# Kernel tuning notes

Measured on AMD Instinct MI355X. Metric: run time of the kernel, lower is better.

The kernel has to match this reference:

```python
import jax, jax.numpy as jnp
import numpy as np

N_VERTEX = 50000
N_EDGE = 400000
HV, HE, P, Q, MV, ME = 128, 64, 3, 3, 128, 128


def setup_inputs() -> dict:
    key = jax.random.key(0)
    ks = jax.random.split(key, 12)
    hv_ftr = jax.random.normal(ks[0], (N_VERTEX, HV), jnp.float32)
    he_ftr = jax.random.normal(ks[1], (N_EDGE, HE), jnp.float32)
    p_ftr = jax.random.normal(ks[2], (N_VERTEX, P), jnp.float32)
    q_ftr = jax.random.normal(ks[3], (N_VERTEX, Q), jnp.float32)
    edge_u = jax.random.randint(ks[4], (N_EDGE,), 0, N_VERTEX, jnp.int32)
    edge_v = jax.random.randint(ks[5], (N_EDGE,), 0, N_VERTEX, jnp.int32)
    # Linear params stored as [in, out] (y = x @ W + b), matching torch Linear math.
    Wa = jax.random.normal(ks[6], (HV, MV), jnp.float32) * 0.05      # attend
    ba = jnp.zeros((MV,), jnp.float32)
    Wal = jax.random.normal(ks[7], (P + Q + HE, 1), jnp.float32) * 0.05  # align
    bal = jnp.zeros((1,), jnp.float32)
    Wl = jax.random.normal(ks[8], (2 * HV + P + Q, ME), jnp.float32) * 0.05  # link
    bl = jnp.zeros((ME,), jnp.float32)
    return dict(hv_ftr=hv_ftr, he_ftr=he_ftr, p_ftr=p_ftr, q_ftr=q_ftr,
                edge_u=edge_u, edge_v=edge_v,
                Wa=Wa, ba=ba, Wal=Wal, bal=bal, Wl=Wl, bl=bl)


def reference(hv_ftr, he_ftr, p_ftr, q_ftr, edge_u, edge_v, Wa, ba, Wal, bal, Wl, bl):
    # dropout is p=0.0 (identity). The dense vew/veb matmuls in the torch code
    # are exactly gathers / a per-vertex (segment) softmax / scatter-adds.
    E = he_ftr.shape[0]
    N = hv_ftr.shape[0]
    # bidirectionalize: vew_u = cat([vew1, vew2]), vew_v = cat([vew2, vew1])
    u = jnp.concatenate([edge_u, edge_v])  # [2E] source of each directed edge
    v = jnp.concatenate([edge_v, edge_u])  # [2E] destination

    hv_u = hv_ftr[u]                       # vew_u.T @ hv_ftr
    hv_v = hv_ftr[v]                       # vew_v.T @ hv_ftr
    p_uv = p_ftr[v] - p_ftr[u]
    q_uv = q_ftr[v] - q_ftr[u]
    he2 = jnp.concatenate([he_ftr, he_ftr], axis=0)

    attend = jax.nn.leaky_relu(hv_v @ Wa + ba)                       # [2E, MV]
    scores = (jnp.concatenate([p_uv, q_uv, he2], axis=1) @ Wal + bal).reshape(-1)  # [2E]

    # per-destination-vertex softmax over incident directed edges
    # (equals dense softmax of vew_v @ diag(scores) + veb_v with -inf mask bias)
    smax = jax.lax.stop_gradient(jax.ops.segment_max(scores, v, num_segments=N))
    ex = jnp.exp(scores - smax[v])
    denom = jax.ops.segment_sum(ex, v, num_segments=N)
    align = ex / denom[v]                                            # [2E]

    mv_ftr = jax.nn.elu(jax.ops.segment_sum(align[:, None] * attend, v, num_segments=N))  # [N, MV]

    me2 = jnp.concatenate([hv_u, p_uv, q_uv, hv_v], axis=1) @ Wl + bl  # [2E, ME]
    me_ftr = jax.nn.leaky_relu(me2[:E] + me2[E:])                      # [E, ME]
    return mv_ftr, me_ftr
```

## Files before the change

kernel.cpp:

```cpp
#include <hip/hip_runtime.h>
#include <math.h>

typedef unsigned short u16;
typedef __attribute__((ext_vector_type(8))) short short8;
typedef __attribute__((ext_vector_type(4))) short short4v;
typedef __attribute__((ext_vector_type(4))) float f32x4;

__device__ __forceinline__ u16 f2b(float f) {
    unsigned u = __float_as_uint(f);
    u += 0x7fffu + ((u >> 16) & 1u);
    return (u16)(u >> 16);
}

__device__ __forceinline__ float b2f(u16 u) {
    return __uint_as_float(((unsigned)u) << 16);
}

__device__ __forceinline__ short8 cvt8(const f32x4* __restrict__ p) {
    f32x4 a = p[0], b = p[1];
    short8 r;
    r[0] = (short)f2b(a[0]); r[1] = (short)f2b(a[1]);
    r[2] = (short)f2b(a[2]); r[3] = (short)f2b(a[3]);
    r[4] = (short)f2b(b[0]); r[5] = (short)f2b(b[1]);
    r[6] = (short)f2b(b[2]); r[7] = (short)f2b(b[3]);
    return r;
}

__global__ __launch_bounds__(256) void k_prep(
    const float* __restrict__ Wa, const float* __restrict__ Wl,
    u16* __restrict__ WpT, u16* __restrict__ WaT,
    unsigned* __restrict__ markw, int nWords, int nbM)
{
    if ((int)blockIdx.x < nbM) {
        int i = (int)blockIdx.x * 256 + (int)threadIdx.x;
        if (i < nWords) markw[i] = 0u;
    } else {
        int c = ((int)blockIdx.x - nbM) * 2 + ((int)threadIdx.x >> 7);
        int k = threadIdx.x & 127;
        WaT[c * 128 + k] = f2b(Wa[k * 128 + c]);
        WpT[c * 128 + k] = f2b(Wl[k * 128 + c] + Wl[(134 + k) * 128 + c]);
    }
}

__global__ void k_mark(const int* __restrict__ eu, const int* __restrict__ ev,
                       unsigned char* __restrict__ mark, int NE)
{
    int i = blockIdx.x * 256 + threadIdx.x;
    if (i < NE) { mark[eu[i]] = 1; mark[ev[i]] = 1; }
}

template<int MODE>
__device__ __forceinline__ void vgemm_body(
    const float* __restrict__ hv, const u16* __restrict__ WT,
    const float* __restrict__ bias, const unsigned char* __restrict__ mark,
    float* __restrict__ out32, u16* __restrict__ outb,
    int NV, int blk)
{
    const int lane = threadIdx.x & 63;
    const int wv   = threadIdx.x >> 6;
    const int m = lane & 15, q = lane >> 4;
    const int n0 = blk * 64 + wv * 16;
    int nl = n0 + m; if (nl >= NV) nl = NV - 1;

    short8 a[4];
    {
        const f32x4* ap = (const f32x4*)(hv + (size_t)nl * 128 + q * 8);
        #pragma unroll
        for (int ks = 0; ks < 4; ++ks) a[ks] = cvt8(ap + ks * 8);
    }

    f32x4 acc[8];
    #pragma unroll
    for (int t = 0; t < 8; ++t) acc[t] = (f32x4){0.f, 0.f, 0.f, 0.f};

    #pragma unroll
    for (int ks = 0; ks < 4; ++ks) {
        #pragma unroll
        for (int t = 0; t < 8; ++t) {
            short8 b = *(const short8*)(WT + (size_t)(t * 16 + m) * 128 + ks * 32 + q * 8);
            acc[t] = __builtin_amdgcn_mfma_f32_16x16x32_bf16(a[ks], b, acc[t], 0, 0, 0);
        }
    }

    #pragma unroll
    for (int t = 0; t < 8; ++t) {
        const int col = t * 16 + m;
        const float bc = bias[col];
        #pragma unroll
        for (int i = 0; i < 4; ++i) {
            const int row = n0 + q * 4 + i;
            if (row < NV) {
                float z = acc[t][i] + bc;
                if (MODE == 0) {
                    float y = (z > 0.f) ? z : 0.01f * z;
                    float r = (y > 0.f) ? y : (__expf(y) - 1.f);
                    if (mark[row] == 0) r = 0.f;
                    __builtin_nontemporal_store(r, &out32[(size_t)row * 128 + col]);
                } else if (MODE == 1) {
                    out32[(size_t)row * 128 + col] = z;
                } else {
                    outb[(size_t)row * 128 + col] = f2b(z);
                }
            }
        }
    }
}

__global__ __launch_bounds__(256) void k_vert(
    const float* __restrict__ hv,
    const u16* __restrict__ WpT, const u16* __restrict__ WaT,
    const float* __restrict__ bl, const float* __restrict__ ba,
    const unsigned char* __restrict__ mark,
    float* __restrict__ mv_out, float* __restrict__ yl32,
    int NV, int nbV)
{
    if ((int)blockIdx.x < nbV)
        vgemm_body<0>(hv, WaT, ba, mark, mv_out, nullptr, NV, (int)blockIdx.x);
    else
        vgemm_body<1>(hv, WpT, bl, nullptr, yl32, nullptr, NV, (int)blockIdx.x - nbV);
}

__global__ __launch_bounds__(256) void k_vmv(
    const float* __restrict__ hv, const u16* __restrict__ WaT,
    const float* __restrict__ ba, const unsigned char* __restrict__ mark,
    float* __restrict__ mv_out, int NV)
{
    vgemm_body<0>(hv, WaT, ba, mark, mv_out, nullptr, NV, (int)blockIdx.x);
}

__global__ __launch_bounds__(256) void k_vylb(
    const float* __restrict__ hv, const u16* __restrict__ WpT,
    const float* __restrict__ bl, u16* __restrict__ ylb, int NV)
{
    vgemm_body<2>(hv, WpT, bl, nullptr, nullptr, ylb, NV, (int)blockIdx.x);
}

__global__ __launch_bounds__(256) void k_edge_f32(
    const float* __restrict__ yl, const int* __restrict__ eu, const int* __restrict__ ev,
    float* __restrict__ me, int NE)
{
    const int lane = threadIdx.x & 63;
    const int wv   = threadIdx.x >> 6;
    const int half = lane >> 5;
    const int c4   = (lane & 31) << 2;
    const int e0   = (int)blockIdx.x * 64 + wv * 16;

    int iu[8], iv[8];
    #pragma unroll
    for (int j = 0; j < 8; ++j) {
        int e = e0 + 2 * j + half; if (e >= NE) e = NE - 1;
        iu[j] = eu[e]; iv[j] = ev[e];
    }
    f32x4 ru[8], rv[8];
    #pragma unroll
    for (int j = 0; j < 8; ++j) {
        ru[j] = *(const f32x4*)(yl + (size_t)iu[j] * 128 + c4);
        rv[j] = *(const f32x4*)(yl + (size_t)iv[j] * 128 + c4);
    }
    #pragma unroll
    for (int j = 0; j < 8; ++j) {
        int e = e0 + 2 * j + half;
        if (e < NE) {
            f32x4 o;
            #pragma unroll
            for (int i = 0; i < 4; ++i) {
                float x = ru[j][i] + rv[j][i];
                o[i] = (x > 0.f) ? x : 0.01f * x;
            }
            __builtin_nontemporal_store(o, (f32x4*)(me + (size_t)e * 128 + c4));
        }
    }
}

__global__ __launch_bounds__(256) void k_edge_b16(
    const u16* __restrict__ ylb, const int* __restrict__ eu, const int* __restrict__ ev,
    float* __restrict__ me, int NE)
{
    const int lane = threadIdx.x & 63;
    const int wv   = threadIdx.x >> 6;
    const int half = lane >> 5;
    const int c4   = (lane & 31) << 2;
    const int e0   = (int)blockIdx.x * 64 + wv * 16;

    int iu[8], iv[8];
    #pragma unroll
    for (int j = 0; j < 8; ++j) {
        int e = e0 + 2 * j + half; if (e >= NE) e = NE - 1;
        iu[j] = eu[e]; iv[j] = ev[e];
    }
    short4v ru[8], rv[8];
    #pragma unroll
    for (int j = 0; j < 8; ++j) {
        ru[j] = *(const short4v*)(ylb + (size_t)iu[j] * 128 + c4);
        rv[j] = *(const short4v*)(ylb + (size_t)iv[j] * 128 + c4);
    }
    #pragma unroll
    for (int j = 0; j < 8; ++j) {
        int e = e0 + 2 * j + half;
        if (e < NE) {
            f32x4 o;
            #pragma unroll
            for (int i = 0; i < 4; ++i) {
                float x = b2f((u16)ru[j][i]) + b2f((u16)rv[j][i]);
                o[i] = (x > 0.f) ? x : 0.01f * x;
            }
            __builtin_nontemporal_store(o, (f32x4*)(me + (size_t)e * 128 + c4));
        }
    }
}

extern "C" void kernel_launch(void* const* d_in, const int* in_sizes, int n_in,
                              void* d_out, int out_size, void* d_ws, size_t ws_size,
                              hipStream_t stream)
{
    const float* hv = (const float*)d_in[0];
    const int*   eu = (const int*)d_in[4];
    const int*   ev = (const int*)d_in[5];
    const float* Wa = (const float*)d_in[6];
    const float* ba = (const float*)d_in[7];
    const float* Wl = (const float*)d_in[10];
    const float* bl = (const float*)d_in[11];

    const int NV = in_sizes[0] / 128;
    const int NE = in_sizes[4];

    float* mv_out = (float*)d_out;
    float* me_out = mv_out + (size_t)NV * 128;

    u16* WpT = (u16*)d_ws;
    u16* WaT = WpT + 128 * 128;
    unsigned char* mark = (unsigned char*)(WaT + 128 * 128);
    const size_t ylOff = 65536 + (((size_t)NV + 255) & ~(size_t)255);

    const int nWords = (NV + 3) / 4;
    const int nbM = (nWords + 255) / 256;
    int nbV = (NV + 63) / 64; if (nbV < 1) nbV = 1;
    int nbE = (NE + 63) / 64; if (nbE < 1) nbE = 1;

    k_prep<<<nbM + 64, 256, 0, stream>>>(Wa, Wl, WpT, WaT, (unsigned*)mark, nWords, nbM);
    k_mark<<<(NE + 255) / 256, 256, 0, stream>>>(eu, ev, mark, NE);

    if (ws_size >= ylOff + (size_t)NV * 512) {
        float* yl32 = (float*)((char*)d_ws + ylOff);
        k_vert<<<2 * nbV, 256, 0, stream>>>(hv, WpT, WaT, bl, ba, mark,
                                            mv_out, yl32, NV, nbV);
        k_edge_f32<<<nbE, 256, 0, stream>>>(yl32, eu, ev, me_out, NE);
    } else if (ws_size >= ylOff + (size_t)NV * 256) {
        u16* ylb = (u16*)((char*)d_ws + ylOff);
        k_vmv<<<nbV, 256, 0, stream>>>(hv, WaT, ba, mark, mv_out, NV);
        k_vylb<<<nbV, 256, 0, stream>>>(hv, WpT, bl, ylb, NV);
        k_edge_b16<<<nbE, 256, 0, stream>>>(ylb, eu, ev, me_out, NE);
    } else {
        u16* ylb = (u16*)mv_out;
        k_vylb<<<nbV, 256, 0, stream>>>(hv, WpT, bl, ylb, NV);
        k_edge_b16<<<nbE, 256, 0, stream>>>(ylb, eu, ev, me_out, NE);
        k_vmv<<<nbV, 256, 0, stream>>>(hv, WaT, ba, mark, mv_out, NV);
    }
}
```

Before: 401.2 us.

## Store link projection in fp16 and co-schedule mv GEMM with edge gather

The per-vertex link projection is now written as fp16 rather than fp32, which halves the table that the edge kernel gathers twice per edge. The mv_ftr attend GEMM now runs in the same launch as the edge gather, with its blocks interleaved proportionally among the edge blocks so the compute-bound and memory-bound work can overlap on the device. This drops a launch and cuts gather bandwidth. In exchange the edge sum carries fp16 rounding and the block-role mapping is more complex.

```diff
diff --git a/kernel.cpp b/kernel.cpp
--- a/kernel.cpp
+++ b/kernel.cpp
@@ -12,8 +12,14 @@
     return (u16)(u >> 16);
 }
 
-__device__ __forceinline__ float b2f(u16 u) {
-    return __uint_as_float(((unsigned)u) << 16);
+__device__ __forceinline__ u16 f2h(float f) {
+    _Float16 h = (_Float16)f;
+    return __builtin_bit_cast(u16, h);
+}
+
+__device__ __forceinline__ float h2f(short s) {
+    _Float16 h = __builtin_bit_cast(_Float16, s);
+    return (float)h;
 }
 
 __device__ __forceinline__ short8 cvt8(const f32x4* __restrict__ p) {
@@ -53,7 +59,7 @@
 __device__ __forceinline__ void vgemm_body(
     const float* __restrict__ hv, const u16* __restrict__ WT,
     const float* __restrict__ bias, const unsigned char* __restrict__ mark,
-    float* __restrict__ out32, u16* __restrict__ outb,
+    float* __restrict__ out32, u16* __restrict__ outh,
     int NV, int blk)
 {
     const int lane = threadIdx.x & 63;
@@ -96,54 +102,30 @@
                     float r = (y > 0.f) ? y : (__expf(y) - 1.f);
                     if (mark[row] == 0) r = 0.f;
                     __builtin_nontemporal_store(r, &out32[(size_t)row * 128 + col]);
-                } else if (MODE == 1) {
-                    out32[(size_t)row * 128 + col] = z;
                 } else {
-                    outb[(size_t)row * 128 + col] = f2b(z);
+                    outh[(size_t)row * 128 + col] = f2h(z);
                 }
             }
         }
     }
 }
 
-__global__ __launch_bounds__(256) void k_vert(
-    const float* __restrict__ hv,
-    const u16* __restrict__ WpT, const u16* __restrict__ WaT,
-    const float* __restrict__ bl, const float* __restrict__ ba,
-    const unsigned char* __restrict__ mark,
-    float* __restrict__ mv_out, float* __restrict__ yl32,
-    int NV, int nbV)
-{
-    if ((int)blockIdx.x < nbV)
-        vgemm_body<0>(hv, WaT, ba, mark, mv_out, nullptr, NV, (int)blockIdx.x);
-    else
-        vgemm_body<1>(hv, WpT, bl, nullptr, yl32, nullptr, NV, (int)blockIdx.x - nbV);
-}
-
-__global__ __launch_bounds__(256) void k_vmv(
-    const float* __restrict__ hv, const u16* __restrict__ WaT,
-    const float* __restrict__ ba, const unsigned char* __restrict__ mark,
-    float* __restrict__ mv_out, int NV)
-{
-    vgemm_body<0>(hv, WaT, ba, mark, mv_out, nullptr, NV, (int)blockIdx.x);
-}
-
-__global__ __launch_bounds__(256) void k_vylb(
+__global__ __launch_bounds__(256) void k_vyl16(
     const float* __restrict__ hv, const u16* __restrict__ WpT,
-    const float* __restrict__ bl, u16* __restrict__ ylb, int NV)
-{
-    vgemm_body<2>(hv, WpT, bl, nullptr, nullptr, ylb, NV, (int)blockIdx.x);
-}
-
-__global__ __launch_bounds__(256) void k_edge_f32(
-    const float* __restrict__ yl, const int* __restrict__ eu, const int* __restrict__ ev,
-    float* __restrict__ me, int NE)
+    const float* __restrict__ bl, u16* __restrict__ ylh, int NV)
+{
+    vgemm_body<3>(hv, WpT, bl, nullptr, nullptr, ylh, NV, (int)blockIdx.x);
+}
+
+__device__ __forceinline__ void edge_body(
+    const u16* __restrict__ ylh, const int* __restrict__ eu, const int* __restrict__ ev,
+    float* __restrict__ me, int NE, int blk)
 {
     const int lane = threadIdx.x & 63;
     const int wv   = threadIdx.x >> 6;
     const int half = lane >> 5;
     const int c4   = (lane & 31) << 2;
-    const int e0   = (int)blockIdx.x * 64 + wv * 16;
+    const int e0   = blk * 64 + wv * 16;
 
     int iu[8], iv[8];
     #pragma unroll
@@ -151,11 +133,11 @@
         int e = e0 + 2 * j + half; if (e >= NE) e = NE - 1;
         iu[j] = eu[e]; iv[j] = ev[e];
     }
-    f32x4 ru[8], rv[8];
+    short4v ru[8], rv[8];
     #pragma unroll
     for (int j = 0; j < 8; ++j) {
-        ru[j] = *(const f32x4*)(yl + (size_t)iu[j] * 128 + c4);
-        rv[j] = *(const f32x4*)(yl + (size_t)iv[j] * 128 + c4);
+        ru[j] = *(const short4v*)(ylh + (size_t)iu[j] * 128 + c4);
+        rv[j] = *(const short4v*)(ylh + (size_t)iv[j] * 128 + c4);
     }
     #pragma unroll
     for (int j = 0; j < 8; ++j) {
@@ -164,7 +146,7 @@
             f32x4 o;
             #pragma unroll
             for (int i = 0; i < 4; ++i) {
-                float x = ru[j][i] + rv[j][i];
+                float x = h2f(ru[j][i]) + h2f(rv[j][i]);
                 o[i] = (x > 0.f) ? x : 0.01f * x;
             }
             __builtin_nontemporal_store(o, (f32x4*)(me + (size_t)e * 128 + c4));
@@ -172,41 +154,21 @@
     }
 }
 
-__global__ __launch_bounds__(256) void k_edge_b16(
-    const u16* __restrict__ ylb, const int* __restrict__ eu, const int* __restrict__ ev,
-    float* __restrict__ me, int NE)
-{
-    const int lane = threadIdx.x & 63;
-    const int wv   = threadIdx.x >> 6;
-    const int half = lane >> 5;
-    const int c4   = (lane & 31) << 2;
-    const int e0   = (int)blockIdx.x * 64 + wv * 16;
-
-    int iu[8], iv[8];
-    #pragma unroll
-    for (int j = 0; j < 8; ++j) {
-        int e = e0 + 2 * j + half; if (e >= NE) e = NE - 1;
-        iu[j] = eu[e]; iv[j] = ev[e];
-    }
-    short4v ru[8], rv[8];
-    #pragma unroll
-    for (int j = 0; j < 8; ++j) {
-        ru[j] = *(const short4v*)(ylb + (size_t)iu[j] * 128 + c4);
-        rv[j] = *(const short4v*)(ylb + (size_t)iv[j] * 128 + c4);
-    }
-    #pragma unroll
-    for (int j = 0; j < 8; ++j) {
-        int e = e0 + 2 * j + half;
-        if (e < NE) {
-            f32x4 o;
-            #pragma unroll
-            for (int i = 0; i < 4; ++i) {
-                float x = b2f((u16)ru[j][i]) + b2f((u16)rv[j][i]);
-                o[i] = (x > 0.f) ? x : 0.01f * x;
-            }
-            __builtin_nontemporal_store(o, (f32x4*)(me + (size_t)e * 128 + c4));
-        }
-    }
+__global__ __launch_bounds__(256) void k_mixed(
+    const u16* __restrict__ ylh, const int* __restrict__ eu, const int* __restrict__ ev,
+    const float* __restrict__ hv, const u16* __restrict__ WaT,
+    const float* __restrict__ ba, const unsigned char* __restrict__ mark,
+    float* __restrict__ mv_out, float* __restrict__ me_out,
+    int NE, int NV, int nbE, int nbV)
+{
+    const unsigned b = blockIdx.x;
+    const unsigned T = (unsigned)nbE + (unsigned)nbV;
+    const unsigned q0 = (b * (unsigned)nbV) / T;
+    const unsigned q1 = ((b + 1u) * (unsigned)nbV) / T;
+    if (q1 > q0)
+        vgemm_body<0>(hv, WaT, ba, mark, mv_out, nullptr, NV, (int)q0);
+    else
+        edge_body(ylh, eu, ev, me_out, NE, (int)(b - q0));
 }
 
 extern "C" void kernel_launch(void* const* d_in, const int* in_sizes, int n_in,
@@ -240,20 +202,17 @@
     k_prep<<<nbM + 64, 256, 0, stream>>>(Wa, Wl, WpT, WaT, (unsigned*)mark, nWords, nbM);
     k_mark<<<(NE + 255) / 256, 256, 0, stream>>>(eu, ev, mark, NE);
 
-    if (ws_size >= ylOff + (size_t)NV * 512) {
-        float* yl32 = (float*)((char*)d_ws + ylOff);
-        k_vert<<<2 * nbV, 256, 0, stream>>>(hv, WpT, WaT, bl, ba, mark,
-                                            mv_out, yl32, NV, nbV);
-        k_edge_f32<<<nbE, 256, 0, stream>>>(yl32, eu, ev, me_out, NE);
-    } else if (ws_size >= ylOff + (size_t)NV * 256) {
-        u16* ylb = (u16*)((char*)d_ws + ylOff);
-        k_vmv<<<nbV, 256, 0, stream>>>(hv, WaT, ba, mark, mv_out, NV);
-        k_vylb<<<nbV, 256, 0, stream>>>(hv, WpT, bl, ylb, NV);
-        k_edge_b16<<<nbE, 256, 0, stream>>>(ylb, eu, ev, me_out, NE);
+    if (ws_size >= ylOff + (size_t)NV * 256) {
+        u16* ylh = (u16*)((char*)d_ws + ylOff);
+        k_vyl16<<<nbV, 256, 0, stream>>>(hv, WpT, bl, ylh, NV);
+        k_mixed<<<nbE + nbV, 256, 0, stream>>>(ylh, eu, ev, hv, WaT, ba, mark,
+                                               mv_out, me_out, NE, NV, nbE, nbV);
     } else {
-        u16* ylb = (u16*)mv_out;
-        k_vylb<<<nbV, 256, 0, stream>>>(hv, WpT, bl, ylb, NV);
-        k_edge_b16<<<nbE, 256, 0, stream>>>(ylb, eu, ev, me_out, NE);
-        k_vmv<<<nbV, 256, 0, stream>>>(hv, WaT, ba, mark, mv_out, NV);
-    }
-}
+        u16* ylh = (u16*)mv_out;
+        k_vyl16<<<nbV, 256, 0, stream>>>(hv, WpT, bl, ylh, NV);
+        k_mixed<<<nbE, 256, 0, stream>>>(ylh, eu, ev, hv, WaT, ba, mark,
+                                         mv_out, me_out, NE, NV, nbE, 0);
+        k_mixed<<<nbV, 256, 0, stream>>>(ylh, eu, ev, hv, WaT, ba, mark,
+                                         mv_out, me_out, NE, NV, 0, nbV);
+    }
+}
```

Result: faster. 366.4 us (-8.7%).
